# Optimization experiments

Hardware: AMD Instinct MI355X
Metric: run time of the kernel (lower is better)

Reference implementation:

```python
import jax, jax.numpy as jnp
import numpy as np

GROUP_SIZE = 64
SCALING = 32.0 / 16.0  # lora_alpha / r


def setup_inputs() -> dict:
    key = jax.random.key(0)
    k = jax.random.split(key, 7)
    B, S, I, O, R = 4, 2048, 4096, 4096, 16
    G = I // GROUP_SIZE
    x = jax.random.normal(k[0], (B, S, I), dtype=jnp.float32)
    W_q = jax.random.randint(k[1], (O, I), 0, 16, dtype=jnp.int32)
    scale = jax.random.uniform(k[2], (O, G), dtype=jnp.float32) * 0.01 + 1e-4
    zero = jax.random.uniform(k[3], (O, G), dtype=jnp.float32) * 8.0
    lora_A = jax.random.normal(k[4], (I, R), dtype=jnp.float32) * 0.02
    lora_B = jax.random.normal(k[5], (R, O), dtype=jnp.float32) * 0.02
    bias = jax.random.normal(k[6], (O,), dtype=jnp.float32) * 0.01
    return {"x": x, "W_q": W_q, "scale": scale, "zero": zero,
            "lora_A": lora_A, "lora_B": lora_B, "bias": bias}


def reference(x, W_q, scale, zero, lora_A, lora_B, bias):
    O, I = W_q.shape
    G = I // GROUP_SIZE
    # HQQ-style group-wise affine dequant: W = (W_q - zero) * scale  -> [O, I]
    Wg = W_q.reshape(O, G, GROUP_SIZE).astype(scale.dtype)
    W = ((Wg - zero[:, :, None]) * scale[:, :, None]).reshape(O, I)
    # base quantized linear: out = x @ W^T
    out = jnp.einsum('bsi,oi->bso', x, W)
    # LoRA low-rank update (dropout is Identity for p=0)
    out = out + (x @ lora_A @ lora_B) * SCALING
    # bias add
    out = out + bias
    return out
```

## Files before the change

kernel.cpp:

```cpp
#include <hip/hip_runtime.h>
#include <hip/hip_bf16.h>
#include <stdint.h>

#define M_DIM 8192
#define N_DIM 4096
#define K_DIM 4096

typedef __attribute__((ext_vector_type(8))) __bf16 bf16x8;
typedef __attribute__((ext_vector_type(4))) float f32x4;

__device__ inline unsigned short f2bf(float f) {
  unsigned u = __builtin_bit_cast(unsigned, f);
  u += 0x7FFF + ((u >> 16) & 1);
  return (unsigned short)(u >> 16);
}

__device__ inline void async_copy16(const void* g, void* l) {
  __builtin_amdgcn_global_load_lds(
      (const __attribute__((address_space(1))) unsigned int*)g,
      (__attribute__((address_space(3))) unsigned int*)l, 16, 0, 0);
}

__global__ __launch_bounds__(256) void prep_kernel(
    const float* __restrict__ x, unsigned short* __restrict__ xb,
    const int* __restrict__ Wq, const float* __restrict__ scale,
    const float* __restrict__ zero, const float* __restrict__ A,
    const float* __restrict__ Bm, unsigned short* __restrict__ Weff) {
  int t = threadIdx.x;
  if (blockIdx.x < 4096) {
    __shared__ float sA[64 * 17];
    __shared__ float sB[16 * 64];
    int bo = blockIdx.x >> 6;
    int bi = blockIdx.x & 63;
    int o0 = bo * 64, i0 = bi * 64;
    for (int j = t; j < 1024; j += 256) sA[(j >> 4) * 17 + (j & 15)] = A[i0 * 16 + j];
    for (int j = t; j < 1024; j += 256) sB[j] = Bm[(j >> 6) * N_DIM + o0 + (j & 63)];
    __syncthreads();
    for (int e = 0; e < 16; ++e) {
      int idx = e * 256 + t;
      int oo = idx >> 6, ii = idx & 63;
      int o = o0 + oo;
      float sc = scale[o * 64 + bi];
      float zp = zero[o * 64 + bi];
      float w = ((float)Wq[(size_t)o * K_DIM + i0 + ii] - zp) * sc;
      float acc = 0.f;
#pragma unroll
      for (int r = 0; r < 16; ++r) acc += sA[ii * 17 + r] * sB[r * 64 + oo];
      w += 2.0f * acc;
      Weff[(size_t)o * K_DIM + i0 + ii] = f2bf(w);
    }
  } else {
    int i = (blockIdx.x - 4096) * 256 + t;
    int stride = 2048 * 256;
    int n4 = (M_DIM * K_DIM) / 4;
    for (; i < n4; i += stride) {
      float4 v = reinterpret_cast<const float4*>(x)[i];
      ushort4 o;
      o.x = f2bf(v.x); o.y = f2bf(v.y); o.z = f2bf(v.z); o.w = f2bf(v.w);
      reinterpret_cast<ushort4*>(xb)[i] = o;
    }
  }
}

#define BAR() __builtin_amdgcn_s_barrier()
#define SB()  __builtin_amdgcn_sched_barrier(0)
#define WAIT_LGKM() do { asm volatile("s_waitcnt lgkmcnt(0)" ::: "memory"); SB(); } while (0)
#define WAIT_VM6()  do { asm volatile("s_waitcnt vmcnt(6)" ::: "memory"); } while (0)

__device__ __forceinline__ bf16x8 lds_frag(const unsigned short* region, int row, int c) {
  return *reinterpret_cast<const bf16x8*>(region + row * 64 + ((c ^ (row & 7)) << 3));
}

__device__ __forceinline__ void readA(const unsigned short* reg, int mh, int lc, int lr,
                                      bf16x8 a[4][2]) {
#pragma unroll
  for (int m = 0; m < 4; ++m) {
    int row = mh * 64 + m * 16 + lc;
#pragma unroll
    for (int kk = 0; kk < 2; ++kk) a[m][kk] = lds_frag(reg, row, kk * 4 + lr);
  }
}

__device__ __forceinline__ void readB(const unsigned short* reg, int nh, int rB, int lc, int lr,
                                      bf16x8 b[2][2]) {
#pragma unroll
  for (int n = 0; n < 2; ++n) {
    int row = rB + (nh * 2 + n) * 16 + lc;
#pragma unroll
    for (int kk = 0; kk < 2; ++kk) b[n][kk] = lds_frag(reg, row, kk * 4 + lr);
  }
}

__device__ __forceinline__ void mfma_quad(const bf16x8 a[4][2], const bf16x8 b[2][2],
                                          f32x4 acc[8][4], int mh, int nh) {
  __builtin_amdgcn_s_setprio(1);
#pragma unroll
  for (int m = 0; m < 4; ++m)
#pragma unroll
    for (int n = 0; n < 2; ++n)
#pragma unroll
      for (int kk = 0; kk < 2; ++kk)
        acc[mh * 4 + m][nh * 2 + n] = __builtin_amdgcn_mfma_f32_16x16x32_bf16(
            a[m][kk], b[n][kk], acc[mh * 4 + m][nh * 2 + n], 0, 0, 0);
  __builtin_amdgcn_s_setprio(0);
}

__global__ __launch_bounds__(512, 2) void gemm_kernel(
    const unsigned short* __restrict__ xb, const unsigned short* __restrict__ wb,
    const float* __restrict__ bias, float* __restrict__ out) {
  __shared__ unsigned short lds[65536];

  int bid = blockIdx.x;
  int swz = (bid & 7) * 64 + (bid >> 3);
  int mt = swz >> 4, nt = swz & 15;
  int m0 = mt * 256, n0 = nt * 256;

  int tid = threadIdx.x;
  int w = tid >> 6, lane = tid & 63;
  int wr = w >> 2, wc = w & 3;
  int lr = lane >> 4, lc = lane & 15;
  int rB = (wc & 1) * 64;

  int r0 = tid >> 3, c0g = (tid & 7) ^ (r0 & 7);
  int ch1 = 512 + tid;
  int r1 = ch1 >> 3, c1g = (ch1 & 7) ^ (r1 & 7);
  int co0 = tid * 8, co1 = ch1 * 8;

  const unsigned short* sA[2][2];
  const unsigned short* sB[2][2];
  sA[0][0] = xb + (size_t)(m0 + r0) * K_DIM + c0g * 8;
  sA[0][1] = xb + (size_t)(m0 + r1) * K_DIM + c1g * 8;
  sA[1][0] = xb + (size_t)(m0 + 128 + r0) * K_DIM + c0g * 8;
  sA[1][1] = xb + (size_t)(m0 + 128 + r1) * K_DIM + c1g * 8;
  sB[0][0] = wb + (size_t)(n0 + r0) * K_DIM + c0g * 8;
  sB[0][1] = wb + (size_t)(n0 + r1) * K_DIM + c1g * 8;
  sB[1][0] = wb + (size_t)(n0 + 128 + r0) * K_DIM + c0g * 8;
  sB[1][1] = wb + (size_t)(n0 + 128 + r1) * K_DIM + c1g * 8;

#define STAGE_A(h, buf, kt) do { \
    async_copy16(sA[h][0] + (kt), &lds[(buf) * 32768 + (h) * 8192 + co0]); \
    async_copy16(sA[h][1] + (kt), &lds[(buf) * 32768 + (h) * 8192 + co1]); } while (0)
#define STAGE_B(h, buf, kt) do { \
    async_copy16(sB[h][0] + (kt), &lds[(buf) * 32768 + 16384 + (h) * 8192 + co0]); \
    async_copy16(sB[h][1] + (kt), &lds[(buf) * 32768 + 16384 + (h) * 8192 + co1]); } while (0)

  const unsigned short* aR[2] = { &lds[wr * 8192], &lds[32768 + wr * 8192] };
  const unsigned short* bR[2] = { &lds[16384 + (wc >> 1) * 8192],
                                  &lds[32768 + 16384 + (wc >> 1) * 8192] };

  f32x4 acc[8][4];
#pragma unroll
  for (int i = 0; i < 8; ++i)
#pragma unroll
    for (int j = 0; j < 4; ++j) acc[i][j] = f32x4{0.f, 0.f, 0.f, 0.f};

  STAGE_A(0, 0, 0); STAGE_B(0, 0, 0); STAGE_B(1, 0, 0); STAGE_A(1, 0, 0);
  STAGE_B(0, 1, 64); STAGE_B(1, 1, 64); STAGE_A(0, 1, 64);
  WAIT_VM6(); BAR(); SB();

  bf16x8 a[4][2], b0[2][2], b1[2][2];

#pragma unroll 1
  for (int i = 0; i < 32; ++i) {
    int k1 = (2 * i + 1) * 64;
    int k2 = ((2 * i + 2) & 63) * 64;
    int k3 = ((2 * i + 3) & 63) * 64;

    readA(aR[0], 0, lc, lr, a); readB(bR[0], 0, rB, lc, lr, b0);
    STAGE_A(1, 1, k1);
    SB(); BAR(); WAIT_LGKM();
    mfma_quad(a, b0, acc, 0, 0);
    SB(); BAR(); SB();
    readB(bR[0], 1, rB, lc, lr, b1);
    SB(); BAR(); WAIT_LGKM();
    mfma_quad(a, b1, acc, 0, 1);
    SB(); BAR(); SB();
    readA(aR[0], 1, lc, lr, a);
    STAGE_B(0, 0, k2);
    SB(); BAR(); WAIT_LGKM();
    mfma_quad(a, b1, acc, 1, 1);
    SB(); BAR(); SB();
    STAGE_B(1, 0, k2); STAGE_A(0, 0, k2);
    SB(); BAR();
    mfma_quad(a, b0, acc, 1, 0);
    SB(); WAIT_VM6(); BAR(); SB();
    readA(aR[1], 0, lc, lr, a); readB(bR[1], 0, rB, lc, lr, b0);
    STAGE_A(1, 0, k2);
    SB(); BAR(); WAIT_LGKM();
    mfma_quad(a, b0, acc, 0, 0);
    SB(); BAR(); SB();
    readB(bR[1], 1, rB, lc, lr, b1);
    SB(); BAR(); WAIT_LGKM();
    mfma_quad(a, b1, acc, 0, 1);
    SB(); BAR(); SB();
    readA(aR[1], 1, lc, lr, a);
    STAGE_B(0, 1, k3);
    SB(); BAR(); WAIT_LGKM();
    mfma_quad(a, b1, acc, 1, 1);
    SB(); BAR(); SB();
    STAGE_B(1, 1, k3); STAGE_A(0, 1, k3);
    SB(); BAR();
    mfma_quad(a, b0, acc, 1, 0);
    SB(); WAIT_VM6(); BAR(); SB();
  }
  asm volatile("s_waitcnt vmcnt(0)" ::: "memory");

#pragma unroll
  for (int ni = 0; ni < 4; ++ni) {
    int n = n0 + wc * 64 + ni * 16 + lc;
    float bv = bias[n];
#pragma unroll
    for (int mi = 0; mi < 8; ++mi) {
      int mb = m0 + wr * 128 + mi * 16 + lr * 4;
#pragma unroll
      for (int j = 0; j < 4; ++j)
        out[(size_t)(mb + j) * N_DIM + n] = acc[mi][ni][j] + bv;
    }
  }
#undef STAGE_A
#undef STAGE_B
}

extern "C" void kernel_launch(void* const* d_in, const int* in_sizes, int n_in,
                              void* d_out, int out_size, void* d_ws, size_t ws_size,
                              hipStream_t stream) {
  const float* x     = (const float*)d_in[0];
  const int*   Wq    = (const int*)d_in[1];
  const float* scale = (const float*)d_in[2];
  const float* zero  = (const float*)d_in[3];
  const float* lA    = (const float*)d_in[4];
  const float* lB    = (const float*)d_in[5];
  const float* bias  = (const float*)d_in[6];
  float* out = (float*)d_out;

  unsigned short* xb = (unsigned short*)d_ws;
  unsigned short* wb = (unsigned short*)((char*)d_ws + (size_t)M_DIM * K_DIM * 2);

  prep_kernel<<<6144, 256, 0, stream>>>(x, xb, Wq, scale, zero, lA, lB, wb);
  gemm_kernel<<<512, 512, 0, stream>>>(xb, wb, bias, out);
}
```

Before: 319.8 us.

## Software-pipeline LDS fragment reads across MFMA phases with double-buffered A registers

Restructures the GEMM main loop so LDS fragment reads for the next sub-tile are issued before the current MFMA block. Two A-register sets (aU and aV) replace the single one, and the explicit lgkmcnt(0) waits are removed so the compiler inserts waits instead. The global prefetch wait is relaxed from vmcnt(6) to vmcnt(2) and placed between half-steps, and the staging pointer arrays are collapsed into two base pointers with offset arithmetic to cut register use. This is meant to hide LDS latency behind matrix ops. The cost is higher VGPR pressure and a subtler ordering of barriers against the async LDS writes.

```diff
diff --git a/kernel.cpp b/kernel.cpp
--- a/kernel.cpp
+++ b/kernel.cpp
@@ -64,8 +64,7 @@
 
 #define BAR() __builtin_amdgcn_s_barrier()
 #define SB()  __builtin_amdgcn_sched_barrier(0)
-#define WAIT_LGKM() do { asm volatile("s_waitcnt lgkmcnt(0)" ::: "memory"); SB(); } while (0)
-#define WAIT_VM6()  do { asm volatile("s_waitcnt vmcnt(6)" ::: "memory"); } while (0)
+#define WAIT_VM2() do { asm volatile("s_waitcnt vmcnt(2)" ::: "memory"); } while (0)
 
 __device__ __forceinline__ bf16x8 lds_frag(const unsigned short* region, int row, int c) {
   return *reinterpret_cast<const bf16x8*>(region + row * 64 + ((c ^ (row & 7)) << 3));
@@ -122,27 +121,19 @@
   int rB = (wc & 1) * 64;
 
   int r0 = tid >> 3, c0g = (tid & 7) ^ (r0 & 7);
-  int ch1 = 512 + tid;
-  int r1 = ch1 >> 3, c1g = (ch1 & 7) ^ (r1 & 7);
-  int co0 = tid * 8, co1 = ch1 * 8;
-
-  const unsigned short* sA[2][2];
-  const unsigned short* sB[2][2];
-  sA[0][0] = xb + (size_t)(m0 + r0) * K_DIM + c0g * 8;
-  sA[0][1] = xb + (size_t)(m0 + r1) * K_DIM + c1g * 8;
-  sA[1][0] = xb + (size_t)(m0 + 128 + r0) * K_DIM + c0g * 8;
-  sA[1][1] = xb + (size_t)(m0 + 128 + r1) * K_DIM + c1g * 8;
-  sB[0][0] = wb + (size_t)(n0 + r0) * K_DIM + c0g * 8;
-  sB[0][1] = wb + (size_t)(n0 + r1) * K_DIM + c1g * 8;
-  sB[1][0] = wb + (size_t)(n0 + 128 + r0) * K_DIM + c0g * 8;
-  sB[1][1] = wb + (size_t)(n0 + 128 + r1) * K_DIM + c1g * 8;
+  int co0 = tid * 8, co1 = (512 + tid) * 8;
+
+  const unsigned short* sA00 = xb + (size_t)(m0 + r0) * K_DIM + c0g * 8;
+  const unsigned short* sB00 = wb + (size_t)(n0 + r0) * K_DIM + c0g * 8;
 
 #define STAGE_A(h, buf, kt) do { \
-    async_copy16(sA[h][0] + (kt), &lds[(buf) * 32768 + (h) * 8192 + co0]); \
-    async_copy16(sA[h][1] + (kt), &lds[(buf) * 32768 + (h) * 8192 + co1]); } while (0)
+    const unsigned short* _p = sA00 + (size_t)(h) * 128 * K_DIM + (size_t)(kt); \
+    async_copy16(_p, &lds[(buf) * 32768 + (h) * 8192 + co0]); \
+    async_copy16(_p + (size_t)64 * K_DIM, &lds[(buf) * 32768 + (h) * 8192 + co1]); } while (0)
 #define STAGE_B(h, buf, kt) do { \
-    async_copy16(sB[h][0] + (kt), &lds[(buf) * 32768 + 16384 + (h) * 8192 + co0]); \
-    async_copy16(sB[h][1] + (kt), &lds[(buf) * 32768 + 16384 + (h) * 8192 + co1]); } while (0)
+    const unsigned short* _p = sB00 + (size_t)(h) * 128 * K_DIM + (size_t)(kt); \
+    async_copy16(_p, &lds[(buf) * 32768 + 16384 + (h) * 8192 + co0]); \
+    async_copy16(_p + (size_t)64 * K_DIM, &lds[(buf) * 32768 + 16384 + (h) * 8192 + co1]); } while (0)
 
   const unsigned short* aR[2] = { &lds[wr * 8192], &lds[32768 + wr * 8192] };
   const unsigned short* bR[2] = { &lds[16384 + (wc >> 1) * 8192],
@@ -154,11 +145,15 @@
 #pragma unroll
     for (int j = 0; j < 4; ++j) acc[i][j] = f32x4{0.f, 0.f, 0.f, 0.f};
 
-  STAGE_A(0, 0, 0); STAGE_B(0, 0, 0); STAGE_B(1, 0, 0); STAGE_A(1, 0, 0);
-  STAGE_B(0, 1, 64); STAGE_B(1, 1, 64); STAGE_A(0, 1, 64);
-  WAIT_VM6(); BAR(); SB();
-
-  bf16x8 a[4][2], b0[2][2], b1[2][2];
+  STAGE_B(0, 0, 0); STAGE_B(1, 0, 0); STAGE_A(0, 0, 0); STAGE_A(1, 0, 0);
+  STAGE_B(0, 1, 64);
+  STAGE_B(1, 1, 64); STAGE_A(0, 1, 64);
+  asm volatile("s_waitcnt vmcnt(6)" ::: "memory");
+  BAR(); SB();
+
+  bf16x8 aU[4][2], aV[4][2], b0[2][2], b1[2][2];
+  readA(aR[0], 0, lc, lr, aU); readB(bR[0], 0, rB, lc, lr, b0);
+  SB();
 
 #pragma unroll 1
   for (int i = 0; i < 32; ++i) {
@@ -166,44 +161,38 @@
     int k2 = ((2 * i + 2) & 63) * 64;
     int k3 = ((2 * i + 3) & 63) * 64;
 
-    readA(aR[0], 0, lc, lr, a); readB(bR[0], 0, rB, lc, lr, b0);
-    STAGE_A(1, 1, k1);
-    SB(); BAR(); WAIT_LGKM();
-    mfma_quad(a, b0, acc, 0, 0);
-    SB(); BAR(); SB();
     readB(bR[0], 1, rB, lc, lr, b1);
-    SB(); BAR(); WAIT_LGKM();
-    mfma_quad(a, b1, acc, 0, 1);
-    SB(); BAR(); SB();
-    readA(aR[0], 1, lc, lr, a);
-    STAGE_B(0, 0, k2);
-    SB(); BAR(); WAIT_LGKM();
-    mfma_quad(a, b1, acc, 1, 1);
-    SB(); BAR(); SB();
-    STAGE_B(1, 0, k2); STAGE_A(0, 0, k2);
-    SB(); BAR();
-    mfma_quad(a, b0, acc, 1, 0);
-    SB(); WAIT_VM6(); BAR(); SB();
-    readA(aR[1], 0, lc, lr, a); readB(bR[1], 0, rB, lc, lr, b0);
-    STAGE_A(1, 0, k2);
-    SB(); BAR(); WAIT_LGKM();
-    mfma_quad(a, b0, acc, 0, 0);
+    SB(); STAGE_A(1, 1, k1); SB();
+    mfma_quad(aU, b0, acc, 0, 0);
+    SB(); BAR(); SB();
+    readA(aR[0], 1, lc, lr, aV);
+    SB();
+    mfma_quad(aU, b1, acc, 0, 1);
+    SB(); BAR(); SB();
+    SB(); STAGE_B(0, 0, k2); SB();
+    mfma_quad(aV, b0, acc, 1, 0);
+    SB(); WAIT_VM2(); BAR(); SB();
+    readA(aR[1], 0, lc, lr, aU); readB(bR[1], 0, rB, lc, lr, b0);
+    SB(); STAGE_B(1, 0, k2); STAGE_A(0, 0, k2); SB();
+    mfma_quad(aV, b1, acc, 1, 1);
     SB(); BAR(); SB();
     readB(bR[1], 1, rB, lc, lr, b1);
-    SB(); BAR(); WAIT_LGKM();
-    mfma_quad(a, b1, acc, 0, 1);
-    SB(); BAR(); SB();
-    readA(aR[1], 1, lc, lr, a);
-    STAGE_B(0, 1, k3);
-    SB(); BAR(); WAIT_LGKM();
-    mfma_quad(a, b1, acc, 1, 1);
-    SB(); BAR(); SB();
-    STAGE_B(1, 1, k3); STAGE_A(0, 1, k3);
-    SB(); BAR();
-    mfma_quad(a, b0, acc, 1, 0);
-    SB(); WAIT_VM6(); BAR(); SB();
-  }
-  asm volatile("s_waitcnt vmcnt(0)" ::: "memory");
+    SB(); STAGE_A(1, 0, k2); SB();
+    mfma_quad(aU, b0, acc, 0, 0);
+    SB(); BAR(); SB();
+    readA(aR[1], 1, lc, lr, aV);
+    SB();
+    mfma_quad(aU, b1, acc, 0, 1);
+    SB(); BAR(); SB();
+    SB(); STAGE_B(0, 1, k3); SB();
+    mfma_quad(aV, b0, acc, 1, 0);
+    SB(); WAIT_VM2(); BAR(); SB();
+    readA(aR[0], 0, lc, lr, aU); readB(bR[0], 0, rB, lc, lr, b0);
+    SB(); STAGE_B(1, 1, k3); STAGE_A(0, 1, k3); SB();
+    mfma_quad(aV, b1, acc, 1, 1);
+    SB(); BAR(); SB();
+  }
+  asm volatile("s_waitcnt vmcnt(0) lgkmcnt(0)" ::: "memory");
 
 #pragma unroll
   for (int ni = 0; ni < 4; ++ni) {
```

Result: faster. 311.5 us (-2.6%).
